# Performance work log

Hardware: AMD Instinct MI355X
Metric: run time of the kernel (lower is better)

The kernel has to match this reference:

```python
import jax, jax.numpy as jnp
import numpy as np

N, D, H, C, L, G, E = 50000, 128, 128, 40, 3, 4, 800000
GRID = jnp.linspace(-2.0, 2.0, G)          # RBF grid on [-2, 2]
DENOM = 4.0 / (G - 1)                      # (grid_max - grid_min) / (num_grids - 1)


def _layernorm(x, g, b, eps=1e-5):
    m = x.mean(-1, keepdims=True)
    v = x.var(-1, keepdims=True)
    return (x - m) * jax.lax.rsqrt(v + eps) * g + b


def _fkan(x, ln_g, ln_b, sw, bw, bb):
    # FastKANLayer: layernorm -> Gaussian RBF basis -> bias-free spline linear, + silu base update
    xn = _layernorm(x, ln_g, ln_b)
    basis = jnp.exp(-(((xn[..., None] - GRID) / DENOM) ** 2))     # [n, d, G]
    ret = basis.reshape(x.shape[0], -1) @ sw.T                    # [n, out]
    return ret + jax.nn.silu(x) @ bw.T + bb


def _gcn_prop(h, src, dst, n):
    # symmetric GCN normalization with self-loops already appended to src/dst
    deg = jax.ops.segment_sum(jnp.ones(src.shape[0], h.dtype), dst, num_segments=n)
    dis = jnp.where(deg > 0, jax.lax.rsqrt(deg), 0.0)
    norm = dis[src] * dis[dst]                                    # [e]
    return jax.ops.segment_sum(h[src] * norm[:, None], dst, num_segments=n)


def _batchnorm(x, g, b, eps=1e-5):
    m = x.mean(0)
    v = x.var(0)  # biased variance, as torch BN uses for normalization
    return (x - m) * jax.lax.rsqrt(v + eps) * g + b


def setup_inputs() -> dict:
    key = jax.random.key(0)
    ks = jax.random.split(key, 8)
    x = jax.random.normal(ks[0], (N, D), jnp.float32)
    edge_index = jax.random.randint(ks[1], (2, E), 0, N, jnp.int64)
    return {
        "x": x,
        "edge_index": edge_index,
        "ln_g": jnp.ones((L, D), jnp.float32),
        "ln_b": jnp.zeros((L, D), jnp.float32),
        "sw": jax.random.normal(ks[2], (L, H, D * G), jnp.float32) * 0.1,
        "bw": jax.random.normal(ks[3], (L, H, D), jnp.float32) * (1.0 / np.sqrt(D)),
        "bb": jnp.zeros((L, H), jnp.float32),
        "gcn_bias": jnp.zeros((L, H), jnp.float32),
        "bn_g": jnp.ones((L, H), jnp.float32),
        "bn_b": jnp.zeros((L, H), jnp.float32),
        "ln_g_out": jnp.ones((D + L * H,), jnp.float32),
        "ln_b_out": jnp.zeros((D + L * H,), jnp.float32),
        "sw_out": jax.random.normal(ks[4], (C, (D + L * H) * G), jnp.float32) * 0.1,
        "bw_out": jax.random.normal(ks[5], (C, D + L * H), jnp.float32) * (1.0 / np.sqrt(D + L * H)),
        "bb_out": jnp.zeros((C,), jnp.float32),
    }


def reference(x, edge_index, ln_g, ln_b, sw, bw, bb, gcn_bias, bn_g, bn_b,
              ln_g_out, ln_b_out, sw_out, bw_out, bb_out):
    loops = jnp.arange(N, dtype=edge_index.dtype)
    src = jnp.concatenate([edge_index[0], loops])
    dst = jnp.concatenate([edge_index[1], loops])
    feats = [x]
    h = x
    for i in range(L):  # fixed small layer count
        h = _fkan(h, ln_g[i], ln_b[i], sw[i], bw[i], bb[i])
        h = _gcn_prop(h, src, dst, N) + gcn_bias[i]
        h = _batchnorm(h, bn_g[i], bn_b[i])
        feats.append(h)
    xcat = jnp.concatenate(feats, axis=1)  # [N, D + L*H] skip-concat
    return _fkan(xcat, ln_g_out, ln_b_out, sw_out, bw_out, bb_out)
```

## Files before the change

### kernel.cpp

```cpp
#include <hip/hip_runtime.h>

#define TPB 256

typedef __attribute__((ext_vector_type(8))) short s8v;
typedef __attribute__((ext_vector_type(4))) float f32x4;
typedef unsigned short u16;

__device__ __forceinline__ u16 f2bf(float f){
  unsigned u = __float_as_uint(f);
  u += 0x7fff + ((u >> 16) & 1);
  return (u16)(u >> 16);
}

__device__ __forceinline__ unsigned pack_bf2(float lo, float hi){
  return (unsigned)f2bf(lo) | ((unsigned)f2bf(hi) << 16);
}

__device__ __forceinline__ float wave_sum(float v){
  #pragma unroll
  for (int off=32; off>0; off>>=1) v += __shfl_xor(v, off, 64);
  return v;
}

__device__ __forceinline__ int wave_incl_scan(int v, int lane){
  #pragma unroll
  for (int off=1; off<64; off<<=1){
    int u = __shfl_up(v, off, 64);
    if (lane >= off) v += u;
  }
  return v;
}

__global__ __launch_bounds__(TPB) void count_k(const int* __restrict__ dstE, int* __restrict__ cnt, int E){
  int e = blockIdx.x*TPB + threadIdx.x;
  if (e < E) atomicAdd(&cnt[dstE[e]], 1);
}

__global__ __launch_bounds__(TPB) void dis_k(const int* __restrict__ cnt, float* __restrict__ disp, int nN){
  int n = blockIdx.x*TPB + threadIdx.x;
  if (n < nN) disp[n] = rsqrtf((float)cnt[n] + 1.0f);
}

__global__ __launch_bounds__(TPB) void scan1_k(const int* __restrict__ cnt, int* __restrict__ rowptr,
                                               int* __restrict__ bsum, int nN){
  int t = threadIdx.x;
  int i = blockIdx.x*TPB + t;
  int lane = t & 63, wid = t >> 6;
  int v = (i < nN) ? cnt[i] : 0;
  int inc = wave_incl_scan(v, lane);
  __shared__ int wsum[4];
  if (lane == 63) wsum[wid] = inc;
  __syncthreads();
  int off = 0;
  #pragma unroll
  for (int w=0; w<4; ++w) if (w < wid) off += wsum[w];
  if (i < nN) rowptr[i] = inc - v + off;
  if (t == 0) bsum[blockIdx.x] = wsum[0]+wsum[1]+wsum[2]+wsum[3];
}

__global__ __launch_bounds__(TPB) void scan2_k(int* __restrict__ bsum, int nbk){
  int t = threadIdx.x;
  int lane = t & 63, wid = t >> 6;
  int v = (t < nbk) ? bsum[t] : 0;
  int inc = wave_incl_scan(v, lane);
  __shared__ int wsum[4];
  if (lane == 63) wsum[wid] = inc;
  __syncthreads();
  int off = 0;
  #pragma unroll
  for (int w=0; w<4; ++w) if (w < wid) off += wsum[w];
  __syncthreads();
  if (t < nbk) bsum[t] = inc - v + off;
}

__global__ __launch_bounds__(TPB) void scan3_k(int* __restrict__ rowptr, const int* __restrict__ bsum, int nN, int E){
  int i = blockIdx.x*TPB + threadIdx.x;
  if (i < nN) rowptr[i] += bsum[blockIdx.x];
  if (i == 0) rowptr[nN] = E;
}

__global__ __launch_bounds__(TPB) void fill_k(const int* __restrict__ srcE, const int* __restrict__ dstE,
                                              const int* __restrict__ rowptr, int* __restrict__ cursor,
                                              int* __restrict__ csr, int E){
  int e = blockIdx.x*TPB + threadIdx.x;
  if (e >= E) return;
  int d = dstE[e];
  int pos = atomicAdd(&cursor[d], 1);
  csr[rowptr[d] + pos] = srcE[e];
}

__global__ __launch_bounds__(TPB) void ln512_k(const float* __restrict__ x, const float* __restrict__ hbuf,
                                               const float* __restrict__ scshAll,
                                               float* __restrict__ meanp, float* __restrict__ rstdp, int nN){
  int g = blockIdx.x*TPB + threadIdx.x;
  int n = g >> 6, lane = g & 63;
  if (n >= nN) return;
  float s = 0.f, sq = 0.f;
  #pragma unroll
  for (int k=0;k<8;k++){
    int d = lane + k*64;
    float v;
    if (d < 128) v = x[(size_t)n*128 + d];
    else {
      int dd = d - 128, li = dd >> 7, cc = dd & 127;
      float raw = hbuf[(size_t)n*384 + dd];
      v = fmaf(raw, scshAll[li*256 + cc], scshAll[li*256 + 128 + cc]);
    }
    s += v; sq += v*v;
  }
  s = wave_sum(s); sq = wave_sum(sq);
  float m = s * (1.f/512.f);
  float var = fmaxf(sq * (1.f/512.f) - m*m, 0.f);
  if (lane == 0){ meanp[n] = m; rstdp[n] = rsqrtf(var + 1e-5f); }
}

__global__ __launch_bounds__(TPB) void prep_wpre_k(const float* __restrict__ sw, const float* __restrict__ bw,
                                                   u16* __restrict__ wpre, int IN, int KSTEPS, int NTILES, int OUTW){
  int idx = blockIdx.x*TPB + threadIdx.x;
  if (idx >= NTILES*KSTEPS*512) return;
  int b = idx & 7, lane = (idx >> 3) & 63, rest = idx >> 9;
  int kstep = rest % KSTEPS, nt = rest / KSTEPS;
  int chunk = kstep / 5, g = kstep % 5;
  int d = chunk*32 + ((lane >> 4)*8 + b);
  int n = nt*16 + (lane & 15);
  float v = 0.f;
  if (n < OUTW) v = (g < 4) ? sw[(size_t)n*IN*4 + d*4 + g] : bw[(size_t)n*IN + d];
  wpre[idx] = f2bf(v);
}

__device__ __forceinline__ void build_frags(const float* __restrict__ h8, float mean, float rstd,
                                            const float* __restrict__ lngv, const float* __restrict__ lnbv,
                                            s8v* __restrict__ a){
  float bas[5][8];
  #pragma unroll
  for (int u=0; u<8; ++u){
    float v = h8[u];
    float xn = (v - mean)*rstd*lngv[u] + lnbv[u];
    float y = 0.75f*xn;
    float z0 = y+1.5f, z1 = y+0.5f, z2 = y-0.5f, z3 = y-1.5f;
    bas[0][u] = __expf(-z0*z0);
    bas[1][u] = __expf(-z1*z1);
    bas[2][u] = __expf(-z2*z2);
    bas[3][u] = __expf(-z3*z3);
    bas[4][u] = v * __builtin_amdgcn_rcpf(1.f + __expf(-v));
  }
  #pragma unroll
  for (int g=0; g<5; ++g){
    #pragma unroll
    for (int j=0; j<4; ++j)
      ((unsigned*)&a[g])[j] = pack_bf2(bas[g][2*j], bas[g][2*j+1]);
  }
}

__global__ __launch_bounds__(TPB) void fkan_layer_k(
    const float* __restrict__ in, int istride,
    const float* __restrict__ scsh,
    const float* __restrict__ lng, const float* __restrict__ lnb,
    const u16* __restrict__ wpre, const float* __restrict__ bias,
    const float* __restrict__ disp, u16* __restrict__ hs, int nN)
{
  const int t = threadIdx.x;
  const int wv = blockIdx.x*(TPB/64) + (t >> 6);
  const int ngrp = (nN + 15) >> 4;
  const int ng = wv >> 1, jh = wv & 1;
  if (ng >= ngrp) return;
  const int l = t & 63, clo = l & 15, kq = l >> 4;
  const int node = ng*16 + clo;
  const int nc = node < nN ? node : nN-1;
  const float* hrow = in + (size_t)nc*istride;

  float h[4][8];
  #pragma unroll
  for (int c=0; c<4; ++c){
    *(float4*)&h[c][0] = *(const float4*)(hrow + c*32 + kq*8);
    *(float4*)&h[c][4] = *(const float4*)(hrow + c*32 + kq*8 + 4);
    if (scsh){
      #pragma unroll
      for (int u=0; u<8; ++u){
        int d = c*32 + kq*8 + u;
        h[c][u] = fmaf(h[c][u], scsh[d], scsh[128 + d]);
      }
    }
  }
  float s = 0.f, sq = 0.f;
  #pragma unroll
  for (int c=0; c<4; ++c)
    #pragma unroll
    for (int u=0; u<8; ++u){ float v = h[c][u]; s += v; sq += v*v; }
  s  += __shfl_xor(s, 16, 64);  s  += __shfl_xor(s, 32, 64);
  sq += __shfl_xor(sq, 16, 64); sq += __shfl_xor(sq, 32, 64);
  float mean = s * (1.f/128.f);
  float var  = fmaxf(sq * (1.f/128.f) - mean*mean, 0.f);
  float rstd = rsqrtf(var + 1e-5f);

  f32x4 acc[4];
  #pragma unroll
  for (int j=0; j<4; ++j) acc[j] = (f32x4)0.f;

  for (int c=0; c<4; ++c){
    float lngv[8], lnbv[8];
    *(float4*)&lngv[0] = *(const float4*)(lng + c*32 + kq*8);
    *(float4*)&lngv[4] = *(const float4*)(lng + c*32 + kq*8 + 4);
    *(float4*)&lnbv[0] = *(const float4*)(lnb + c*32 + kq*8);
    *(float4*)&lnbv[4] = *(const float4*)(lnb + c*32 + kq*8 + 4);
    s8v a[5];
    build_frags(h[c], mean, rstd, lngv, lnbv, a);
    #pragma unroll
    for (int ks=0; ks<5; ++ks){
      const int kglob = c*5 + ks;
      #pragma unroll
      for (int j=0; j<4; ++j){
        s8v b = *(const s8v*)(wpre + ((size_t)((jh*4 + j)*20 + kglob)*64 + l)*8);
        acc[j] = __builtin_amdgcn_mfma_f32_16x16x32_bf16(a[ks], b, acc[j], 0, 0, 0);
      }
    }
  }
  float bv[4];
  #pragma unroll
  for (int j=0; j<4; ++j) bv[j] = bias[(jh*4 + j)*16 + clo];
  #pragma unroll
  for (int rr=0; rr<4; ++rr){
    int nw = ng*16 + kq*4 + rr;
    if (nw < nN){
      float dsc = disp[nw];
      #pragma unroll
      for (int j=0; j<4; ++j)
        hs[(size_t)nw*128 + (jh*4 + j)*16 + clo] = f2bf((acc[j][rr] + bv[j]) * dsc);
    }
  }
}

__global__ __launch_bounds__(TPB) void fkan_out_k(
    const float* __restrict__ x, const float* __restrict__ hbuf,
    const float* __restrict__ scshAll,
    const float* __restrict__ meanp, const float* __restrict__ rstdp,
    const float* __restrict__ lng, const float* __restrict__ lnb,
    const u16* __restrict__ wpre, const float* __restrict__ bias,
    float* __restrict__ out, int nN)
{
  __shared__ float sred[4][24][64];
  const int t = threadIdx.x;
  const int w = t >> 6, l = t & 63, clo = l & 15, kq = l >> 4;
  const int nb0 = blockIdx.x * 32;
  int nc0 = nb0 + clo;      nc0 = nc0 < nN ? nc0 : nN-1;
  int nc1 = nb0 + 16 + clo; nc1 = nc1 < nN ? nc1 : nN-1;
  const float mean0 = meanp[nc0], rstd0 = rstdp[nc0];
  const float mean1 = meanp[nc1], rstd1 = rstdp[nc1];

  f32x4 acc[2][3];
  #pragma unroll
  for (int m=0; m<2; ++m)
    #pragma unroll
    for (int j=0; j<3; ++j) acc[m][j] = (f32x4)0.f;

  #pragma unroll
  for (int cc=0; cc<4; ++cc){
    const int c = w*4 + cc;
    const int d0 = c*32 + kq*8;
    float lngv[8], lnbv[8];
    *(float4*)&lngv[0] = *(const float4*)(lng + d0);
    *(float4*)&lngv[4] = *(const float4*)(lng + d0 + 4);
    *(float4*)&lnbv[0] = *(const float4*)(lnb + d0);
    *(float4*)&lnbv[4] = *(const float4*)(lnb + d0 + 4);
    float h0[8], h1[8];
    if (d0 < 128){
      const float* s0 = x + (size_t)nc0*128 + d0;
      const float* s1 = x + (size_t)nc1*128 + d0;
      *(float4*)&h0[0] = *(const float4*)(s0);  *(float4*)&h0[4] = *(const float4*)(s0+4);
      *(float4*)&h1[0] = *(const float4*)(s1);  *(float4*)&h1[4] = *(const float4*)(s1+4);
    } else {
      int dd = d0 - 128, li = dd >> 7, cc2 = dd & 127;
      const float* s0 = hbuf + (size_t)nc0*384 + dd;
      const float* s1 = hbuf + (size_t)nc1*384 + dd;
      *(float4*)&h0[0] = *(const float4*)(s0);  *(float4*)&h0[4] = *(const float4*)(s0+4);
      *(float4*)&h1[0] = *(const float4*)(s1);  *(float4*)&h1[4] = *(const float4*)(s1+4);
      #pragma unroll
      for (int u=0; u<8; ++u){
        float sc = scshAll[li*256 + cc2 + u], sh = scshAll[li*256 + 128 + cc2 + u];
        h0[u] = fmaf(h0[u], sc, sh);
        h1[u] = fmaf(h1[u], sc, sh);
      }
    }
    s8v a0[5], a1[5];
    build_frags(h0, mean0, rstd0, lngv, lnbv, a0);
    build_frags(h1, mean1, rstd1, lngv, lnbv, a1);
    #pragma unroll
    for (int ks=0; ks<5; ++ks){
      const int kglob = c*5 + ks;
      #pragma unroll
      for (int j=0; j<3; ++j){
        s8v b = *(const s8v*)(wpre + ((size_t)(j*80 + kglob)*64 + l)*8);
        acc[0][j] = __builtin_amdgcn_mfma_f32_16x16x32_bf16(a0[ks], b, acc[0][j], 0, 0, 0);
        acc[1][j] = __builtin_amdgcn_mfma_f32_16x16x32_bf16(a1[ks], b, acc[1][j], 0, 0, 0);
      }
    }
  }
  #pragma unroll
  for (int m=0; m<2; ++m)
    #pragma unroll
    for (int j=0; j<3; ++j)
      #pragma unroll
      for (int rr=0; rr<4; ++rr)
        sred[w][m*12 + j*4 + rr][l] = acc[m][j][rr];
  __syncthreads();
  #pragma unroll
  for (int k=0; k<6; ++k){
    int q = t + k*256;
    int slot = q >> 6, l2 = q & 63;
    float val = sred[0][slot][l2] + sred[1][slot][l2] + sred[2][slot][l2] + sred[3][slot][l2];
    int m = slot >= 12 ? 1 : 0;
    int jrr = slot - m*12;
    int j = jrr >> 2, rr = jrr & 3;
    int nodeq = nb0 + m*16 + (l2 >> 4)*4 + rr;
    int col = j*16 + (l2 & 15);
    if (nodeq < nN && col < 40)
      out[(size_t)nodeq*40 + col] = val + bias[col];
  }
}

__device__ __forceinline__ void acc_bf4(uint2 u, float& a0, float& a1, float& a2, float& a3){
  a0 += __uint_as_float(u.x << 16);
  a1 += __uint_as_float(u.x & 0xffff0000u);
  a2 += __uint_as_float(u.y << 16);
  a3 += __uint_as_float(u.y & 0xffff0000u);
}

__global__ __launch_bounds__(TPB) void gcn_k(const u16* __restrict__ hs, const int* __restrict__ rowptr,
                                             const int* __restrict__ csr, const float* __restrict__ disp,
                                             float* __restrict__ outb, int nN){
  int g = blockIdx.x*TPB + threadIdx.x;
  int n = g >> 6, lane = g & 63;
  if (n >= nN) return;
  const uint2* H2 = (const uint2*)hs;
  const int li = lane & 31, half = lane >> 5;
  int e0 = rowptr[n], e1 = rowptr[n+1];
  float a0=0.f, a1=0.f, a2=0.f, a3=0.f;
  for (int base = e0; base < e1; base += 8){
    int r[4];
    #pragma unroll
    for (int k=0; k<4; ++k){
      int idx = base + half*4 + k;
      int idc = idx < e1 ? idx : e0;
      int rv  = csr[idc];
      r[k] = idx < e1 ? rv : nN;
    }
    #pragma unroll
    for (int k=0; k<4; ++k){
      uint2 u = H2[(size_t)r[k]*32 + li];
      acc_bf4(u, a0, a1, a2, a3);
    }
  }
  a0 += __shfl_xor(a0, 32, 64);
  a1 += __shfl_xor(a1, 32, 64);
  a2 += __shfl_xor(a2, 32, 64);
  a3 += __shfl_xor(a3, 32, 64);
  if (half == 0){
    uint2 u = H2[(size_t)n*32 + li];
    acc_bf4(u, a0, a1, a2, a3);
    float dn = disp[n];
    float4 r4; r4.x = a0*dn; r4.y = a1*dn; r4.z = a2*dn; r4.w = a3*dn;
    *(float4*)(outb + (size_t)n*384 + li*4) = r4;
  }
}

__global__ __launch_bounds__(TPB) void bn_stat_k(const float* __restrict__ hb, float* __restrict__ stats, int nN){
  int col  = threadIdx.x & 127;
  int half = threadIdx.x >> 7;
  float s=0.f, sq=0.f;
  for (int r = blockIdx.x*2 + half; r < nN; r += gridDim.x*2){
    float v = hb[(size_t)r*384 + col];
    s += v; sq += v*v;
  }
  __shared__ float ls[TPB], lq[TPB];
  ls[threadIdx.x]=s; lq[threadIdx.x]=sq;
  __syncthreads();
  if (half==0){
    s  = ls[threadIdx.x] + ls[threadIdx.x+128];
    sq = lq[threadIdx.x] + lq[threadIdx.x+128];
    atomicAdd(&stats[col], s);
    atomicAdd(&stats[128+col], sq);
  }
}

__global__ void bn_fin_k(const float* __restrict__ stats, const float* __restrict__ g, const float* __restrict__ b,
                         float* __restrict__ scsh, int nN){
  int c = threadIdx.x;
  float inv = 1.f/(float)nN;
  float m = stats[c]*inv;
  float var = fmaxf(stats[128+c]*inv - m*m, 0.f);
  float sc = g[c]*rsqrtf(var + 1e-5f);
  scsh[c] = sc;
  scsh[128+c] = b[c] - m*sc;
}

extern "C" void kernel_launch(void* const* d_in, const int* in_sizes, int n_in,
                              void* d_out, int out_size, void* d_ws, size_t ws_size,
                              hipStream_t stream)
{
  const float* x        = (const float*)d_in[0];
  const int*   ei       = (const int*)d_in[1];
  const float* ln_g     = (const float*)d_in[2];
  const float* ln_b     = (const float*)d_in[3];
  const float* sw       = (const float*)d_in[4];
  const float* bw       = (const float*)d_in[5];
  const float* bb       = (const float*)d_in[6];
  const float* bn_g     = (const float*)d_in[8];
  const float* bn_b     = (const float*)d_in[9];
  const float* ln_g_out = (const float*)d_in[10];
  const float* ln_b_out = (const float*)d_in[11];
  const float* sw_out   = (const float*)d_in[12];
  const float* bw_out   = (const float*)d_in[13];
  const float* bb_out   = (const float*)d_in[14];
  float* out = (float*)d_out;

  const int nN = in_sizes[0] / 128;
  const int E  = in_sizes[1] / 2;

  char* ws = (char*)d_ws;
  size_t off = 0;
  auto alloc = [&](size_t bytes)->char*{
    char* p = ws + off; off = (off + bytes + 255) & ~size_t(255); return p;
  };
  float* hbuf  = (float*)alloc((size_t)nN*384*4);
  u16*   hs    = (u16*)alloc((size_t)(nN+1)*128*2);
  float* meanp = (float*)alloc((size_t)nN*4);
  float* rstdp = (float*)alloc((size_t)nN*4);
  float* disp  = (float*)alloc((size_t)nN*4);
  float* stats = (float*)alloc(256*4);
  float* scshL = (float*)alloc(3*256*4);
  u16*   wpreL = (u16*)alloc((size_t)3*8*20*512*2);
  u16*   wpreO = (u16*)alloc((size_t)3*80*512*2);
  int* cnt     = (int*)alloc((size_t)nN*4);
  int* cursor  = (int*)alloc((size_t)nN*4);
  int* rowptr  = (int*)alloc((size_t)(nN+1)*4);
  int* bsum    = (int*)alloc(256*4);
  int* csr     = (int*)alloc((size_t)E*4);
  (void)ws_size; (void)n_in; (void)out_size;

  const int* srcE = ei;
  const int* dstE = ei + E;

  hipMemsetAsync(cnt, 0, (size_t)nN*4, stream);
  hipMemsetAsync(cursor, 0, (size_t)nN*4, stream);
  hipMemsetAsync(hs + (size_t)nN*128, 0, 256, stream);

  for (int i=0; i<3; ++i)
    prep_wpre_k<<<(8*20*512 + TPB-1)/TPB, TPB, 0, stream>>>(
        sw + (size_t)i*128*512, bw + (size_t)i*128*128, wpreL + (size_t)i*8*20*512, 128, 20, 8, 128);
  prep_wpre_k<<<(3*80*512 + TPB-1)/TPB, TPB, 0, stream>>>(
      sw_out, bw_out, wpreO, 512, 80, 3, 40);

  const int nbE = (E + TPB-1)/TPB;
  const int nbN = (nN + TPB-1)/TPB;
  count_k<<<nbE, TPB, 0, stream>>>(dstE, cnt, E);
  dis_k<<<nbN, TPB, 0, stream>>>(cnt, disp, nN);
  scan1_k<<<nbN, TPB, 0, stream>>>(cnt, rowptr, bsum, nN);
  scan2_k<<<1, TPB, 0, stream>>>(bsum, nbN);
  scan3_k<<<nbN, TPB, 0, stream>>>(rowptr, bsum, nN, E);
  fill_k<<<nbE, TPB, 0, stream>>>(srcE, dstE, rowptr, cursor, csr, E);

  const int nbW = (nN*64 + TPB-1)/TPB;
  const int nbL = (((nN + 15)/16)*2 + 3)/4;
  const int nbO = (nN + 31)/32;

  for (int i=0; i<3; ++i){
    const float* inbase = (i==0) ? x : (hbuf + (size_t)(i-1)*128);
    int instride = (i==0) ? 128 : 384;
    const float* scsh_in = (i==0) ? (const float*)nullptr : (scshL + (size_t)(i-1)*256);
    fkan_layer_k<<<nbL, TPB, 0, stream>>>(
        inbase, instride, scsh_in, ln_g + (size_t)i*128, ln_b + (size_t)i*128,
        wpreL + (size_t)i*8*20*512, bb + (size_t)i*128, disp, hs, nN);
    gcn_k<<<nbW, TPB, 0, stream>>>(hs, rowptr, csr, disp, hbuf + (size_t)i*128, nN);
    hipMemsetAsync(stats, 0, 256*4, stream);
    bn_stat_k<<<256, TPB, 0, stream>>>(hbuf + (size_t)i*128, stats, nN);
    bn_fin_k<<<1, 128, 0, stream>>>(stats, bn_g + (size_t)i*128, bn_b + (size_t)i*128,
                                    scshL + (size_t)i*256, nN);
  }

  ln512_k<<<nbW, TPB, 0, stream>>>(x, hbuf, scshL, meanp, rstdp, nN);
  fkan_out_k<<<nbO, TPB, 0, stream>>>(
      x, hbuf, scshL, meanp, rstdp, ln_g_out, ln_b_out, wpreO, bb_out, out, nN);
}
```

Before: 484.8 us.

## Store GCN layer outputs as bf16 in per-layer planar buffers

The GCN aggregation output, previously an fp32 interleaved [N,384] buffer, is now written as bf16 into three separate [N,128] planes. Every consumer (next layer's FKAN, BN stats, the 512-wide layernorm and the output FKAN) reads and unpacks bf16, which roughly halves the intermediate traffic. BN statistics are now computed on bf16-rounded values with a 4-stream, column-pair reduction. The cost is an extra rounding of pre-BN activations, which could shift accuracy.

```diff
diff --git a/kernel.cpp b/kernel.cpp
--- a/kernel.cpp
+++ b/kernel.cpp
@@ -1,4 +1,5 @@
 #include <hip/hip_runtime.h>
+#include <hip/hip_bf16.h>
 
 #define TPB 256
 
@@ -7,14 +8,17 @@
 typedef unsigned short u16;
 
 __device__ __forceinline__ u16 f2bf(float f){
-  unsigned u = __float_as_uint(f);
-  u += 0x7fff + ((u >> 16) & 1);
-  return (u16)(u >> 16);
+  union { __hip_bfloat16 h; u16 u; } cv;
+  cv.h = __float2bfloat16(f);
+  return cv.u;
 }
 
 __device__ __forceinline__ unsigned pack_bf2(float lo, float hi){
   return (unsigned)f2bf(lo) | ((unsigned)f2bf(hi) << 16);
 }
+
+__device__ __forceinline__ float bflo(unsigned u){ return __uint_as_float(u << 16); }
+__device__ __forceinline__ float bfhi(unsigned u){ return __uint_as_float(u & 0xffff0000u); }
 
 __device__ __forceinline__ float wave_sum(float v){
   #pragma unroll
@@ -89,7 +93,7 @@
   csr[rowptr[d] + pos] = srcE[e];
 }
 
-__global__ __launch_bounds__(TPB) void ln512_k(const float* __restrict__ x, const float* __restrict__ hbuf,
+__global__ __launch_bounds__(TPB) void ln512_k(const float* __restrict__ x, const u16* __restrict__ hl16,
                                                const float* __restrict__ scshAll,
                                                float* __restrict__ meanp, float* __restrict__ rstdp, int nN){
   int g = blockIdx.x*TPB + threadIdx.x;
@@ -98,12 +102,13 @@
   float s = 0.f, sq = 0.f;
   #pragma unroll
   for (int k=0;k<8;k++){
-    int d = lane + k*64;
     float v;
-    if (d < 128) v = x[(size_t)n*128 + d];
-    else {
-      int dd = d - 128, li = dd >> 7, cc = dd & 127;
-      float raw = hbuf[(size_t)n*384 + dd];
+    if (k < 2){
+      v = x[(size_t)n*128 + lane + k*64];
+    } else {
+      int k2 = k - 2, li = k2 >> 1, cc = lane + (k2&1)*64;
+      float raw = bflo((unsigned)hl16[((size_t)li*nN + n)*128 + cc] << 0) ;
+      raw = __uint_as_float(((unsigned)hl16[((size_t)li*nN + n)*128 + cc]) << 16);
       v = fmaf(raw, scshAll[li*256 + cc], scshAll[li*256 + 128 + cc]);
     }
     s += v; sq += v*v;
@@ -152,8 +157,9 @@
   }
 }
 
+template<bool BF16IN>
 __global__ __launch_bounds__(TPB) void fkan_layer_k(
-    const float* __restrict__ in, int istride,
+    const float* __restrict__ in32, const u16* __restrict__ in16,
     const float* __restrict__ scsh,
     const float* __restrict__ lng, const float* __restrict__ lnb,
     const u16* __restrict__ wpre, const float* __restrict__ bias,
@@ -167,19 +173,25 @@
   const int l = t & 63, clo = l & 15, kq = l >> 4;
   const int node = ng*16 + clo;
   const int nc = node < nN ? node : nN-1;
-  const float* hrow = in + (size_t)nc*istride;
 
   float h[4][8];
   #pragma unroll
   for (int c=0; c<4; ++c){
-    *(float4*)&h[c][0] = *(const float4*)(hrow + c*32 + kq*8);
-    *(float4*)&h[c][4] = *(const float4*)(hrow + c*32 + kq*8 + 4);
-    if (scsh){
+    if (BF16IN){
+      uint4 raw = *(const uint4*)(in16 + (size_t)nc*128 + c*32 + kq*8);
+      h[c][0]=bflo(raw.x); h[c][1]=bfhi(raw.x);
+      h[c][2]=bflo(raw.y); h[c][3]=bfhi(raw.y);
+      h[c][4]=bflo(raw.z); h[c][5]=bfhi(raw.z);
+      h[c][6]=bflo(raw.w); h[c][7]=bfhi(raw.w);
       #pragma unroll
       for (int u=0; u<8; ++u){
         int d = c*32 + kq*8 + u;
         h[c][u] = fmaf(h[c][u], scsh[d], scsh[128 + d]);
       }
+    } else {
+      const float* hrow = in32 + (size_t)nc*128;
+      *(float4*)&h[c][0] = *(const float4*)(hrow + c*32 + kq*8);
+      *(float4*)&h[c][4] = *(const float4*)(hrow + c*32 + kq*8 + 4);
     }
   }
   float s = 0.f, sq = 0.f;
@@ -231,7 +243,7 @@
 }
 
 __global__ __launch_bounds__(TPB) void fkan_out_k(
-    const float* __restrict__ x, const float* __restrict__ hbuf,
+    const float* __restrict__ x, const u16* __restrict__ hl16,
     const float* __restrict__ scshAll,
     const float* __restrict__ meanp, const float* __restrict__ rstdp,
     const float* __restrict__ lng, const float* __restrict__ lnb,
@@ -270,10 +282,12 @@
       *(float4*)&h1[0] = *(const float4*)(s1);  *(float4*)&h1[4] = *(const float4*)(s1+4);
     } else {
       int dd = d0 - 128, li = dd >> 7, cc2 = dd & 127;
-      const float* s0 = hbuf + (size_t)nc0*384 + dd;
-      const float* s1 = hbuf + (size_t)nc1*384 + dd;
-      *(float4*)&h0[0] = *(const float4*)(s0);  *(float4*)&h0[4] = *(const float4*)(s0+4);
-      *(float4*)&h1[0] = *(const float4*)(s1);  *(float4*)&h1[4] = *(const float4*)(s1+4);
+      uint4 r0 = *(const uint4*)(hl16 + ((size_t)li*nN + nc0)*128 + cc2);
+      uint4 r1 = *(const uint4*)(hl16 + ((size_t)li*nN + nc1)*128 + cc2);
+      h0[0]=bflo(r0.x); h0[1]=bfhi(r0.x); h0[2]=bflo(r0.y); h0[3]=bfhi(r0.y);
+      h0[4]=bflo(r0.z); h0[5]=bfhi(r0.z); h0[6]=bflo(r0.w); h0[7]=bfhi(r0.w);
+      h1[0]=bflo(r1.x); h1[1]=bfhi(r1.x); h1[2]=bflo(r1.y); h1[3]=bfhi(r1.y);
+      h1[4]=bflo(r1.z); h1[5]=bfhi(r1.z); h1[6]=bflo(r1.w); h1[7]=bfhi(r1.w);
       #pragma unroll
       for (int u=0; u<8; ++u){
         float sc = scshAll[li*256 + cc2 + u], sh = scshAll[li*256 + 128 + cc2 + u];
@@ -319,15 +333,13 @@
 }
 
 __device__ __forceinline__ void acc_bf4(uint2 u, float& a0, float& a1, float& a2, float& a3){
-  a0 += __uint_as_float(u.x << 16);
-  a1 += __uint_as_float(u.x & 0xffff0000u);
-  a2 += __uint_as_float(u.y << 16);
-  a3 += __uint_as_float(u.y & 0xffff0000u);
+  a0 += bflo(u.x); a1 += bfhi(u.x);
+  a2 += bflo(u.y); a3 += bfhi(u.y);
 }
 
 __global__ __launch_bounds__(TPB) void gcn_k(const u16* __restrict__ hs, const int* __restrict__ rowptr,
                                              const int* __restrict__ csr, const float* __restrict__ disp,
-                                             float* __restrict__ outb, int nN){
+                                             u16* __restrict__ hl, int nN){
   int g = blockIdx.x*TPB + threadIdx.x;
   int n = g >> 6, lane = g & 63;
   if (n >= nN) return;
@@ -358,27 +370,35 @@
     uint2 u = H2[(size_t)n*32 + li];
     acc_bf4(u, a0, a1, a2, a3);
     float dn = disp[n];
-    float4 r4; r4.x = a0*dn; r4.y = a1*dn; r4.z = a2*dn; r4.w = a3*dn;
-    *(float4*)(outb + (size_t)n*384 + li*4) = r4;
-  }
-}
-
-__global__ __launch_bounds__(TPB) void bn_stat_k(const float* __restrict__ hb, float* __restrict__ stats, int nN){
-  int col  = threadIdx.x & 127;
-  int half = threadIdx.x >> 7;
-  float s=0.f, sq=0.f;
-  for (int r = blockIdx.x*2 + half; r < nN; r += gridDim.x*2){
-    float v = hb[(size_t)r*384 + col];
-    s += v; sq += v*v;
-  }
-  __shared__ float ls[TPB], lq[TPB];
-  ls[threadIdx.x]=s; lq[threadIdx.x]=sq;
+    uint2 o;
+    o.x = pack_bf2(a0*dn, a1*dn);
+    o.y = pack_bf2(a2*dn, a3*dn);
+    *(uint2*)(hl + (size_t)n*128 + li*4) = o;
+  }
+}
+
+__global__ __launch_bounds__(TPB) void bn_stat_k(const u16* __restrict__ hl, float* __restrict__ stats, int nN){
+  int cp   = threadIdx.x & 63;
+  int strm = threadIdx.x >> 6;
+  const unsigned* H = (const unsigned*)hl;
+  float s0=0.f, s1=0.f, q0=0.f, q1=0.f;
+  for (int r = blockIdx.x*4 + strm; r < nN; r += gridDim.x*4){
+    unsigned u = H[(size_t)r*64 + cp];
+    float lo = bflo(u), hi = bfhi(u);
+    s0 += lo; q0 += lo*lo; s1 += hi; q1 += hi*hi;
+  }
+  __shared__ float ls[4][64][4];
+  ls[strm][cp][0] = s0; ls[strm][cp][1] = q0; ls[strm][cp][2] = s1; ls[strm][cp][3] = q1;
   __syncthreads();
-  if (half==0){
-    s  = ls[threadIdx.x] + ls[threadIdx.x+128];
-    sq = lq[threadIdx.x] + lq[threadIdx.x+128];
-    atomicAdd(&stats[col], s);
-    atomicAdd(&stats[128+col], sq);
+  if (strm == 0){
+    float S0 = ls[0][cp][0]+ls[1][cp][0]+ls[2][cp][0]+ls[3][cp][0];
+    float Q0 = ls[0][cp][1]+ls[1][cp][1]+ls[2][cp][1]+ls[3][cp][1];
+    float S1 = ls[0][cp][2]+ls[1][cp][2]+ls[2][cp][2]+ls[3][cp][2];
+    float Q1 = ls[0][cp][3]+ls[1][cp][3]+ls[2][cp][3]+ls[3][cp][3];
+    atomicAdd(&stats[cp*2],       S0);
+    atomicAdd(&stats[cp*2+1],     S1);
+    atomicAdd(&stats[128+cp*2],   Q0);
+    atomicAdd(&stats[128+cp*2+1], Q1);
   }
 }
 
@@ -421,7 +441,7 @@
   auto alloc = [&](size_t bytes)->char*{
     char* p = ws + off; off = (off + bytes + 255) & ~size_t(255); return p;
   };
-  float* hbuf  = (float*)alloc((size_t)nN*384*4);
+  u16*   hl16  = (u16*)alloc((size_t)3*nN*128*2);
   u16*   hs    = (u16*)alloc((size_t)(nN+1)*128*2);
   float* meanp = (float*)alloc((size_t)nN*4);
   float* rstdp = (float*)alloc((size_t)nN*4);
@@ -464,20 +484,24 @@
   const int nbO = (nN + 31)/32;
 
   for (int i=0; i<3; ++i){
-    const float* inbase = (i==0) ? x : (hbuf + (size_t)(i-1)*128);
-    int instride = (i==0) ? 128 : 384;
-    const float* scsh_in = (i==0) ? (const float*)nullptr : (scshL + (size_t)(i-1)*256);
-    fkan_layer_k<<<nbL, TPB, 0, stream>>>(
-        inbase, instride, scsh_in, ln_g + (size_t)i*128, ln_b + (size_t)i*128,
-        wpreL + (size_t)i*8*20*512, bb + (size_t)i*128, disp, hs, nN);
-    gcn_k<<<nbW, TPB, 0, stream>>>(hs, rowptr, csr, disp, hbuf + (size_t)i*128, nN);
+    if (i == 0){
+      fkan_layer_k<false><<<nbL, TPB, 0, stream>>>(
+          x, (const u16*)nullptr, (const float*)nullptr,
+          ln_g, ln_b, wpreL, bb, disp, hs, nN);
+    } else {
+      fkan_layer_k<true><<<nbL, TPB, 0, stream>>>(
+          (const float*)nullptr, hl16 + (size_t)(i-1)*nN*128, scshL + (size_t)(i-1)*256,
+          ln_g + (size_t)i*128, ln_b + (size_t)i*128,
+          wpreL + (size_t)i*8*20*512, bb + (size_t)i*128, disp, hs, nN);
+    }
+    gcn_k<<<nbW, TPB, 0, stream>>>(hs, rowptr, csr, disp, hl16 + (size_t)i*nN*128, nN);
     hipMemsetAsync(stats, 0, 256*4, stream);
-    bn_stat_k<<<256, TPB, 0, stream>>>(hbuf + (size_t)i*128, stats, nN);
+    bn_stat_k<<<256, TPB, 0, stream>>>(hl16 + (size_t)i*nN*128, stats, nN);
     bn_fin_k<<<1, 128, 0, stream>>>(stats, bn_g + (size_t)i*128, bn_b + (size_t)i*128,
                                     scshL + (size_t)i*256, nN);
   }
 
-  ln512_k<<<nbW, TPB, 0, stream>>>(x, hbuf, scshL, meanp, rstdp, nN);
+  ln512_k<<<nbW, TPB, 0, stream>>>(x, hl16, scshL, meanp, rstdp, nN);
   fkan_out_k<<<nbO, TPB, 0, stream>>>(
-      x, hbuf, scshL, meanp, rstdp, ln_g_out, ln_b_out, wpreO, bb_out, out, nN);
-}
+      x, hl16, scshL, meanp, rstdp, ln_g_out, ln_b_out, wpreO, bb_out, out, nN);
+}
```

New measurement: 456.1 us. 1.06x faster.
